# Performance work log

Measured on AMD Instinct MI355X. Metric: run time of the kernel, lower is better.

## Reference

```python
import jax, jax.numpy as jnp
import numpy as np

STRIDE = 4.0      # fpn_strides[0]
POOL = 7          # roi_align_size
SR = 2            # roi_align_sampling_ratio
NUM_CLASSES = 10
B, N = 2, 512
C, H, W = 256, 256, 256
OUT = 1024


def _bilinear(feat_hwc, y, x):
    # feat_hwc: [H, W, C]; y, x: [N, 7, 7, SR, SR] sample coords (feature units)
    Hf, Wf, _ = feat_hwc.shape
    valid = (y > -1.0) & (y < Hf) & (x > -1.0) & (x < Wf)
    y = jnp.clip(y, 0.0, Hf - 1.0)
    x = jnp.clip(x, 0.0, Wf - 1.0)
    y0 = jnp.floor(y)
    x0 = jnp.floor(x)
    y0i = y0.astype(jnp.int32)
    x0i = x0.astype(jnp.int32)
    y1i = jnp.minimum(y0i + 1, Hf - 1)
    x1i = jnp.minimum(x0i + 1, Wf - 1)
    ly = (y - y0)[..., None]
    lx = (x - x0)[..., None]
    hy = 1.0 - ly
    hx = 1.0 - lx
    v = (hy * hx * feat_hwc[y0i, x0i] + hy * lx * feat_hwc[y0i, x1i]
         + ly * hx * feat_hwc[y1i, x0i] + ly * lx * feat_hwc[y1i, x1i])
    return v * valid[..., None]


def _roi_align_rotated(feat_hwc, boxes):
    # boxes: [N, 5] = (cx, cy, w, h, theta) in feature coords -> [N, 7, 7, C]
    cx, cy, w, h, th = (boxes[:, k] for k in range(5))
    bins = jnp.arange(POOL, dtype=feat_hwc.dtype)
    sub = (jnp.arange(SR, dtype=feat_hwc.dtype) + 0.5) / SR
    # local (box-frame) coords of sample points along each axis: [N, 7, SR]
    ys = -h[:, None, None] / 2 + (h / POOL)[:, None, None] * (bins[None, :, None] + sub[None, None, :])
    xs = -w[:, None, None] / 2 + (w / POOL)[:, None, None] * (bins[None, :, None] + sub[None, None, :])
    yy = ys[:, :, None, :, None]  # [N,7,1,SR,1]
    xx = xs[:, None, :, None, :]  # [N,1,7,1,SR]
    cos = jnp.cos(th)[:, None, None, None, None]
    sin = jnp.sin(th)[:, None, None, None, None]
    gx = cx[:, None, None, None, None] + xx * cos - yy * sin
    gy = cy[:, None, None, None, None] + xx * sin + yy * cos
    v = _bilinear(feat_hwc, gy, gx)  # [N,7,7,SR,SR,C]
    return v.mean(axis=(3, 4))       # average-pool the SRxSR samples per bin


def norm_angle(a):
    return (a + jnp.pi / 2) % jnp.pi - jnp.pi / 2


def setup_inputs():
    key = jax.random.key(0)
    ks = jax.random.split(key, 14)
    feat = jax.random.normal(ks[0], (B, C, H, W), jnp.float32)
    cx = jax.random.uniform(ks[1], (B, N), minval=16.0, maxval=H - 16.0)
    cy = jax.random.uniform(ks[2], (B, N), minval=16.0, maxval=W - 16.0)
    bw = jax.random.uniform(ks[3], (B, N), minval=8.0, maxval=64.0)
    bh = jax.random.uniform(ks[4], (B, N), minval=8.0, maxval=64.0)
    th = jax.random.uniform(ks[5], (B, N), minval=-np.pi / 2, maxval=np.pi / 2)
    proposals = jnp.stack([cx, cy, bw, bh, th], axis=-1).astype(jnp.float32)
    d_in = C * POOL * POOL
    s = 0.02
    return {
        'feat': feat,
        'proposals': proposals,
        'W1': jax.random.normal(ks[6], (d_in, OUT), jnp.float32) * s,
        'b1': jnp.zeros((OUT,), jnp.float32),
        'W2': jax.random.normal(ks[7], (OUT, OUT), jnp.float32) * s,
        'b2': jnp.zeros((OUT,), jnp.float32),
        'Wcls': jax.random.normal(ks[8], (OUT, NUM_CLASSES + 1), jnp.float32) * s,
        'bcls': jnp.zeros((NUM_CLASSES + 1,), jnp.float32),
        'Wreg': jax.random.normal(ks[9], (OUT, 5), jnp.float32) * s,
        'breg': jnp.zeros((5,), jnp.float32),
    }


def reference(feat, proposals, W1, b1, W2, b2, Wcls, bcls, Wreg, breg):
    Bn, Nn = proposals.shape[:2]
    feat_hwc = jnp.transpose(feat, (0, 2, 3, 1))  # [B,H,W,C]
    pooled = jax.vmap(_roi_align_rotated)(feat_hwc, proposals)  # [B,N,7,7,C]
    # torch flattens [N, C, 7, 7] -> C*49; match that layout
    x = jnp.transpose(pooled, (0, 1, 4, 2, 3)).reshape(Bn, Nn, -1)
    x = jax.nn.relu(x @ W1 + b1)
    x = jax.nn.relu(x @ W2 + b2)
    cls = x @ Wcls + bcls   # [B,N,11]
    reg = x @ Wreg + breg   # [B,N,5]
    # decode (proposals scaled to image coords by stride; theta unscaled)
    scale = jnp.array([STRIDE, STRIDE, STRIDE, STRIDE, 1.0], feat.dtype)
    p = proposals * scale
    clamp_v = float(abs(np.log(16.0 / 1000.0)))
    bx = p[..., 2] * reg[..., 0] + p[..., 0]
    by = p[..., 3] * reg[..., 1] + p[..., 1]
    bw = p[..., 2] * jnp.exp(jnp.clip(reg[..., 2], -clamp_v, clamp_v))
    bh = p[..., 3] * jnp.exp(jnp.clip(reg[..., 3], -clamp_v, clamp_v))
    ba = norm_angle(p[..., 4] + reg[..., 4])
    boxes = jnp.stack([bx, by, bw, bh, ba], axis=-1)
    return boxes, cls
```

## Files before the change

kernel.cpp:

```cpp
#include <hip/hip_runtime.h>
#include <math.h>
#include <stdint.h>

#define BB 2
#define NN 512
#define CC 256
#define HH 256
#define WW 256
#define DIN 12544
#define OUT1 1024
#define NCLS 11
#define NROI 1024
#define SK1 8
#define SK2 2

typedef short bf16x8 __attribute__((ext_vector_type(8)));
typedef float f32x4 __attribute__((ext_vector_type(4)));

__device__ inline unsigned short f2bf(float f) {
  unsigned int u = __float_as_uint(f);
  u += 0x7FFF + ((u >> 16) & 1);
  return (unsigned short)(u >> 16);
}
__device__ inline float bf2f(unsigned short h) {
  return __uint_as_float(((unsigned int)h) << 16);
}
__device__ inline float4 ld_bf4(const unsigned short* p) {
  ushort4 r = *(const ushort4*)p;
  return make_float4(bf2f(r.x), bf2f(r.y), bf2f(r.z), bf2f(r.w));
}

__device__ inline void gll16(const void* g, void* l) {
  __builtin_amdgcn_global_load_lds(
      reinterpret_cast<const __attribute__((address_space(1))) void*>(
          reinterpret_cast<uintptr_t>(g)),
      reinterpret_cast<__attribute__((address_space(3))) void*>(
          (unsigned int)reinterpret_cast<uintptr_t>(l)),
      16, 0, 0);
}

__global__ __launch_bounds__(256) void prep_kernel(
    const float* __restrict__ feat, unsigned short* __restrict__ fhwc,
    const float* __restrict__ W1, unsigned short* __restrict__ W1T,
    const float* __restrict__ W2, unsigned short* __restrict__ W2T,
    int n_tr) {
  __shared__ float tile[8320];
  int bid = blockIdx.x;
  int tid = threadIdx.x;

  if (bid < n_tr) {
    int hw0 = (bid & 511) * 128;
    int c0 = ((bid >> 9) & 3) * 64;
    int b = bid >> 11;
    int cl_base = tid >> 5;
    int hwq = (tid & 31) * 4;
#pragma unroll
    for (int pass = 0; pass < 8; ++pass) {
      int cl = cl_base + pass * 8;
      float4 v = *(const float4*)(feat +
                                  ((size_t)b * CC + c0 + cl) * (HH * WW) +
                                  hw0 + hwq);
      tile[(hwq + 0) * 65 + cl] = v.x;
      tile[(hwq + 1) * 65 + cl] = v.y;
      tile[(hwq + 2) * 65 + cl] = v.z;
      tile[(hwq + 3) * 65 + cl] = v.w;
    }
    __syncthreads();
    int hi = tid >> 4, lo = tid & 15;
#pragma unroll
    for (int pass = 0; pass < 8; ++pass) {
      int hwl = hi + pass * 16;
      int cc = lo * 4;
      ushort4 o;
      o.x = f2bf(tile[hwl * 65 + cc + 0]);
      o.y = f2bf(tile[hwl * 65 + cc + 1]);
      o.z = f2bf(tile[hwl * 65 + cc + 2]);
      o.w = f2bf(tile[hwl * 65 + cc + 3]);
      *(ushort4*)(fhwc + ((size_t)b * (HH * WW) + hw0 + hwl) * CC + c0 + cc) =
          o;
    }
    return;
  }

  int u = bid - n_tr;
  const float* in;
  unsigned short* out;
  int Kout, kblk, nblk;
  bool perm;
  if (u < 1568) {
    in = W1; out = W1T; Kout = DIN; kblk = u % 196; nblk = u / 196; perm = true;
  } else {
    u -= 1568;
    in = W2; out = W2T; Kout = OUT1; kblk = u & 15; nblk = u >> 4; perm = false;
  }
  int k0 = kblk * 64, n0 = nblk * 128;
  int kl_base = tid >> 5;
  int nq = (tid & 31) * 4;
#pragma unroll
  for (int pass = 0; pass < 8; ++pass) {
    int kl = kl_base + pass * 8;
    int k = k0 + kl;
    int row = perm ? ((k & 255) * 49 + (k >> 8)) : k;
    float4 v = *(const float4*)(in + (size_t)row * OUT1 + n0 + nq);
    tile[kl * 129 + nq + 0] = v.x;
    tile[kl * 129 + nq + 1] = v.y;
    tile[kl * 129 + nq + 2] = v.z;
    tile[kl * 129 + nq + 3] = v.w;
  }
  __syncthreads();
  int hi = tid >> 4, lo = tid & 15;
#pragma unroll
  for (int pass = 0; pass < 8; ++pass) {
    int nl = hi + pass * 16;
    int kq = lo * 4;
    ushort4 o;
    o.x = f2bf(tile[(kq + 0) * 129 + nl]);
    o.y = f2bf(tile[(kq + 1) * 129 + nl]);
    o.z = f2bf(tile[(kq + 2) * 129 + nl]);
    o.w = f2bf(tile[(kq + 3) * 129 + nl]);
    *(ushort4*)(out + (size_t)(n0 + nl) * Kout + k0 + kq) = o;
  }
}

__device__ inline void bilin(float gy, float gx, int& y0, int& x0, int& y1,
                             int& x1, float& w00, float& w01, float& w10,
                             float& w11) {
  float valid = (gy > -1.f && gy < 256.f && gx > -1.f && gx < 256.f) ? 0.25f : 0.f;
  float y = fminf(fmaxf(gy, 0.f), 255.f);
  float x = fminf(fmaxf(gx, 0.f), 255.f);
  float yf = floorf(y), xf = floorf(x);
  y0 = (int)yf; x0 = (int)xf;
  y1 = min(y0 + 1, 255); x1 = min(x0 + 1, 255);
  float ly = y - yf, lx = x - xf, hy = 1.f - ly, hx = 1.f - lx;
  w00 = hy * hx * valid; w01 = hy * lx * valid;
  w10 = ly * hx * valid; w11 = ly * lx * valid;
}

__global__ __launch_bounds__(256) void roi_align_hwc(
    const unsigned short* __restrict__ fhwc, const float* __restrict__ props,
    unsigned short* __restrict__ pooled) {
  int roi = blockIdx.x >> 1;
  int half = blockIdx.x & 1;
  int b = roi >> 9;
  const float* p = props + (size_t)roi * 5;
  float cx = p[0], cy = p[1], w = p[2], h = p[3], th = p[4];
  float sn = sinf(th), cs = cosf(th);
  int wave = threadIdx.x >> 6, lane = threadIdx.x & 63;
  int c4 = lane * 4;
  const unsigned short* fb = fhwc + (size_t)b * HH * WW * CC;
  unsigned short* outp = pooled + (size_t)roi * DIN;

  for (int bin = half * 4 + wave; bin < 49; bin += 8) {
    int py = bin / 7, px = bin - py * 7;
    float a0 = 0.f, a1 = 0.f, a2 = 0.f, a3 = 0.f;
#pragma unroll
    for (int sy = 0; sy < 2; ++sy) {
#pragma unroll
      for (int sx = 0; sx < 2; ++sx) {
        float ys = -0.5f * h + (h / 7.0f) * ((float)py + ((float)sy + 0.5f) * 0.5f);
        float xs = -0.5f * w + (w / 7.0f) * ((float)px + ((float)sx + 0.5f) * 0.5f);
        float gx = cx + xs * cs - ys * sn;
        float gy = cy + xs * sn + ys * cs;
        int y0, x0, y1, x1; float w00, w01, w10, w11;
        bilin(gy, gx, y0, x0, y1, x1, w00, w01, w10, w11);
        float4 v00 = ld_bf4(fb + ((size_t)(y0 * WW + x0)) * CC + c4);
        float4 v01 = ld_bf4(fb + ((size_t)(y0 * WW + x1)) * CC + c4);
        float4 v10 = ld_bf4(fb + ((size_t)(y1 * WW + x0)) * CC + c4);
        float4 v11 = ld_bf4(fb + ((size_t)(y1 * WW + x1)) * CC + c4);
        a0 += w00 * v00.x + w01 * v01.x + w10 * v10.x + w11 * v11.x;
        a1 += w00 * v00.y + w01 * v01.y + w10 * v10.y + w11 * v11.y;
        a2 += w00 * v00.z + w01 * v01.z + w10 * v10.z + w11 * v11.z;
        a3 += w00 * v00.w + w01 * v01.w + w10 * v10.w + w11 * v11.w;
      }
    }
    ushort4 o;
    o.x = f2bf(a0); o.y = f2bf(a1); o.z = f2bf(a2); o.w = f2bf(a3);
    *(ushort4*)(outp + bin * 256 + c4) = o;
  }
}

__global__ __launch_bounds__(256) void roi_align_nchw(
    const float* __restrict__ feat, const float* __restrict__ props,
    unsigned short* __restrict__ pooled) {
  int roi = blockIdx.x;
  int b = roi >> 9;
  int c = threadIdx.x;
  const float* p = props + (size_t)roi * 5;
  float cx = p[0], cy = p[1], w = p[2], h = p[3], th = p[4];
  float sn = sinf(th), cs = cosf(th);
  const float* fb = feat + ((size_t)b * CC + c) * (HH * WW);
  unsigned short* outp = pooled + (size_t)roi * DIN;
  for (int bin = 0; bin < 49; ++bin) {
    int py = bin / 7, px = bin - py * 7;
    float acc = 0.f;
#pragma unroll
    for (int sy = 0; sy < 2; ++sy) {
#pragma unroll
      for (int sx = 0; sx < 2; ++sx) {
        float ys = -0.5f * h + (h / 7.0f) * ((float)py + ((float)sy + 0.5f) * 0.5f);
        float xs = -0.5f * w + (w / 7.0f) * ((float)px + ((float)sx + 0.5f) * 0.5f);
        float gx = cx + xs * cs - ys * sn;
        float gy = cy + xs * sn + ys * cs;
        int y0, x0, y1, x1; float w00, w01, w10, w11;
        bilin(gy, gx, y0, x0, y1, x1, w00, w01, w10, w11);
        acc += w00 * fb[(size_t)y0 * WW + x0] + w01 * fb[(size_t)y0 * WW + x1] +
               w10 * fb[(size_t)y1 * WW + x0] + w11 * fb[(size_t)y1 * WW + x1];
      }
    }
    outp[bin * 256 + c] = f2bf(acc);
  }
}

__global__ __launch_bounds__(256) void gemm_mfma_128(
    const unsigned short* __restrict__ A, const unsigned short* __restrict__ Bw,
    float* __restrict__ part, int K, int Ks) {
  __shared__ short As[128 * 32];
  __shared__ short Bs[128 * 32];
  int tid = threadIdx.x;
  int w = tid >> 6, lane = tid & 63;
  int quad = lane >> 4, l16 = lane & 15;
  int m0 = blockIdx.y * 128, n0 = blockIdx.x * 128;
  int bz = blockIdx.z;
  int wm = w >> 1, wn = w & 1;

  const char* pA = (const char*)A +
      ((size_t)(m0 + 32 * w + (lane >> 2)) * K + (size_t)bz * Ks) * 2 +
      (lane & 3) * 16;
  const char* pB = (const char*)Bw +
      ((size_t)(n0 + 32 * w + (lane >> 2)) * K + (size_t)bz * Ks) * 2 +
      (lane & 3) * 16;
  short* la = &As[w * 1024];
  short* lb = &Bs[w * 1024];
  const size_t rstep = (size_t)K * 2 * 16;

  f32x4 acc[4][4] = {};
  int aoff[4], boff[4];
#pragma unroll
  for (int t = 0; t < 4; ++t) {
    aoff[t] = (wm * 64 + t * 16 + l16) * 32 + quad * 8;
    boff[t] = (wn * 64 + t * 16 + l16) * 32 + quad * 8;
  }

  for (int kk = 0; kk < Ks; kk += 32) {
    __syncthreads();
    gll16(pA, la);
    gll16(pA + rstep, la + 512);
    gll16(pB, lb);
    gll16(pB + rstep, lb + 512);
    pA += 64; pB += 64;
    __syncthreads();
    bf16x8 af[4], bfr[4];
#pragma unroll
    for (int t = 0; t < 4; ++t) af[t] = *(const bf16x8*)&As[aoff[t]];
#pragma unroll
    for (int t = 0; t < 4; ++t) bfr[t] = *(const bf16x8*)&Bs[boff[t]];
#pragma unroll
    for (int mt = 0; mt < 4; ++mt)
#pragma unroll
      for (int nt = 0; nt < 4; ++nt)
        acc[mt][nt] = __builtin_amdgcn_mfma_f32_16x16x32_bf16(
            af[mt], bfr[nt], acc[mt][nt], 0, 0, 0);
  }

  float* pp = part + (size_t)bz * (OUT1 * NROI);
#pragma unroll
  for (int mt = 0; mt < 4; ++mt)
#pragma unroll
    for (int nt = 0; nt < 4; ++nt) {
      int col = n0 + wn * 64 + nt * 16 + l16;
#pragma unroll
      for (int r = 0; r < 4; ++r) {
        int row = m0 + wm * 64 + mt * 16 + quad * 4 + r;
        pp[(size_t)row * OUT1 + col] = acc[mt][nt][r];
      }
    }
}

__global__ __launch_bounds__(256) void reduce_relu_bf16(
    const float* __restrict__ part, const float* __restrict__ bias,
    unsigned short* __restrict__ out) {
  int i = blockIdx.x * 256 + threadIdx.x;
  int base = i * 4;
  int col = base & (OUT1 - 1);
  const float4* p = (const float4*)part;
  float4 s = p[i];
#pragma unroll
  for (int z = 1; z < SK1; ++z) {
    float4 t = p[i + (size_t)z * (NROI * OUT1 / 4)];
    s.x += t.x; s.y += t.y; s.z += t.z; s.w += t.w;
  }
  float4 bv = *(const float4*)(bias + col);
  ushort4 o;
  o.x = f2bf(fmaxf(s.x + bv.x, 0.f));
  o.y = f2bf(fmaxf(s.y + bv.y, 0.f));
  o.z = f2bf(fmaxf(s.z + bv.z, 0.f));
  o.w = f2bf(fmaxf(s.w + bv.w, 0.f));
  *(ushort4*)(out + base) = o;
}

__global__ __launch_bounds__(256) void gemm_mfma_64_part(
    const unsigned short* __restrict__ A, const unsigned short* __restrict__ Bw,
    float* __restrict__ part, int K, int Ks) {
  __shared__ short As[64 * 64];
  __shared__ short Bs[64 * 64];
  int tid = threadIdx.x;
  int w = tid >> 6, lane = tid & 63;
  int quad = lane >> 4, l16 = lane & 15;
  int m0 = blockIdx.y * 64, n0 = blockIdx.x * 64;
  int bz = blockIdx.z;
  int wm = w >> 1, wn = w & 1;

  const char* pA = (const char*)A +
      ((size_t)(m0 + 16 * w + (lane >> 3)) * K + (size_t)bz * Ks) * 2 +
      (lane & 7) * 16;
  const char* pB = (const char*)Bw +
      ((size_t)(n0 + 16 * w + (lane >> 3)) * K + (size_t)bz * Ks) * 2 +
      (lane & 7) * 16;
  short* la = &As[w * 1024];
  short* lb = &Bs[w * 1024];
  const size_t rstep = (size_t)K * 2 * 8;

  f32x4 acc[2][2] = {};
  int aoff[2], boff[2];
#pragma unroll
  for (int t = 0; t < 2; ++t) {
    aoff[t] = (wm * 32 + t * 16 + l16) * 64 + quad * 8;
    boff[t] = (wn * 32 + t * 16 + l16) * 64 + quad * 8;
  }

  for (int kk = 0; kk < Ks; kk += 64) {
    __syncthreads();
    gll16(pA, la);
    gll16(pA + rstep, la + 512);
    gll16(pB, lb);
    gll16(pB + rstep, lb + 512);
    pA += 128; pB += 128;
    __syncthreads();
#pragma unroll
    for (int ks = 0; ks < 2; ++ks) {
      bf16x8 af[2], bfr[2];
#pragma unroll
      for (int t = 0; t < 2; ++t) af[t] = *(const bf16x8*)&As[aoff[t] + ks * 32];
#pragma unroll
      for (int t = 0; t < 2; ++t) bfr[t] = *(const bf16x8*)&Bs[boff[t] + ks * 32];
#pragma unroll
      for (int mt = 0; mt < 2; ++mt)
#pragma unroll
        for (int nt = 0; nt < 2; ++nt)
          acc[mt][nt] = __builtin_amdgcn_mfma_f32_16x16x32_bf16(
              af[mt], bfr[nt], acc[mt][nt], 0, 0, 0);
    }
  }
  float* pp = part + (size_t)bz * (OUT1 * NROI);
#pragma unroll
  for (int mt = 0; mt < 2; ++mt)
#pragma unroll
    for (int nt = 0; nt < 2; ++nt) {
      int col = n0 + wn * 32 + nt * 16 + l16;
#pragma unroll
      for (int r = 0; r < 4; ++r) {
        int row = m0 + wm * 32 + mt * 16 + quad * 4 + r;
        pp[(size_t)row * OUT1 + col] = acc[mt][nt][r];
      }
    }
}

__global__ __launch_bounds__(256) void head_kernel(
    const float* __restrict__ P0, const float* __restrict__ P1,
    const float* __restrict__ b2, const float* __restrict__ Wcls,
    const float* __restrict__ bcls, const float* __restrict__ Wreg,
    const float* __restrict__ breg, const float* __restrict__ props,
    float* __restrict__ out) {
  __shared__ float xrow[1024];
  __shared__ float partial[16][17];
  __shared__ float res[16];
  int row = blockIdx.x;
  int tid = threadIdx.x;
  {
    size_t off = (size_t)row * 1024 + tid * 4;
    float4 a = *(const float4*)(P0 + off);
    float4 b = *(const float4*)(P1 + off);
    float4 bv = *(const float4*)(b2 + tid * 4);
    xrow[tid * 4 + 0] = fmaxf(a.x + b.x + bv.x, 0.f);
    xrow[tid * 4 + 1] = fmaxf(a.y + b.y + bv.y, 0.f);
    xrow[tid * 4 + 2] = fmaxf(a.z + b.z + bv.z, 0.f);
    xrow[tid * 4 + 3] = fmaxf(a.w + b.w + bv.w, 0.f);
  }
  __syncthreads();
  int col = tid & 15, slice = tid >> 4;
  float s = 0.f;
  if (col < NCLS) {
    for (int k = slice * 64; k < slice * 64 + 64; ++k)
      s += xrow[k] * Wcls[(size_t)k * NCLS + col];
  } else {
    int rc = col - NCLS;
    for (int k = slice * 64; k < slice * 64 + 64; ++k)
      s += xrow[k] * Wreg[(size_t)k * 5 + rc];
  }
  partial[slice][col] = s;
  __syncthreads();
  if (tid < 16) {
    float t = 0.f;
    for (int sl = 0; sl < 16; ++sl) t += partial[sl][tid];
    t += (tid < NCLS) ? bcls[tid] : breg[tid - NCLS];
    res[tid] = t;
  }
  __syncthreads();
  if (tid < NCLS) out[5120 + (size_t)row * NCLS + tid] = res[tid];
  if (tid == 0) {
    const float* p = props + (size_t)row * 5;
    float p0 = p[0] * 4.f, p1 = p[1] * 4.f, p2 = p[2] * 4.f, p3 = p[3] * 4.f,
          p4 = p[4];
    float r0 = res[11], r1 = res[12], r2 = res[13], r3 = res[14], r4 = res[15];
    const float V = 4.135166556742356f;
    float bx = p2 * r0 + p0;
    float by = p3 * r1 + p1;
    float bw = p2 * expf(fminf(fmaxf(r2, -V), V));
    float bh = p3 * expf(fminf(fmaxf(r3, -V), V));
    const float PI = 3.14159265358979323846f;
    float a = p4 + r4;
    float m = fmodf(a + PI * 0.5f, PI);
    if (m < 0.f) m += PI;
    float ba = m - PI * 0.5f;
    float* bo = out + (size_t)row * 5;
    bo[0] = bx; bo[1] = by; bo[2] = bw; bo[3] = bh; bo[4] = ba;
  }
}

extern "C" void kernel_launch(void* const* d_in, const int* in_sizes, int n_in,
                              void* d_out, int out_size, void* d_ws,
                              size_t ws_size, hipStream_t stream) {
  const float* feat  = (const float*)d_in[0];
  const float* props = (const float*)d_in[1];
  const float* W1    = (const float*)d_in[2];
  const float* b1    = (const float*)d_in[3];
  const float* W2    = (const float*)d_in[4];
  const float* b2    = (const float*)d_in[5];
  const float* Wcls  = (const float*)d_in[6];
  const float* bcls  = (const float*)d_in[7];
  const float* Wreg  = (const float*)d_in[8];
  const float* breg  = (const float*)d_in[9];
  float* out = (float*)d_out;

  char* wp = (char*)d_ws;
  unsigned short* pooled = (unsigned short*)wp; wp += (size_t)NROI * DIN * 2;
  unsigned short* W1T    = (unsigned short*)wp; wp += (size_t)OUT1 * DIN * 2;
  unsigned short* W2T    = (unsigned short*)wp; wp += (size_t)OUT1 * OUT1 * 2;
  unsigned short* x1     = (unsigned short*)wp; wp += (size_t)NROI * OUT1 * 2;
  float*          part1  = (float*)wp;          wp += (size_t)SK1 * NROI * OUT1 * 4;
  float*          part2  = (float*)wp;          wp += (size_t)SK2 * NROI * OUT1 * 4;
  unsigned short* fhwc   = (unsigned short*)wp;

  size_t need_min  = (size_t)(wp - (char*)d_ws);
  size_t need_full = need_min + (size_t)BB * CC * HH * WW * 2;

  int n_tr = (ws_size >= need_full) ? (BB * 4 * (HH * WW / 128)) : 0;
  int n_prep = n_tr + 1568 + 128;

  prep_kernel<<<n_prep, 256, 0, stream>>>(feat, fhwc, W1, W1T, W2, W2T, n_tr);

  if (n_tr) {
    roi_align_hwc<<<NROI * 2, 256, 0, stream>>>(fhwc, props, pooled);
  } else {
    roi_align_nchw<<<NROI, 256, 0, stream>>>(feat, props, pooled);
  }

  gemm_mfma_128<<<dim3(8, 8, SK1), 256, 0, stream>>>(pooled, W1T, part1, DIN,
                                                     DIN / SK1);
  reduce_relu_bf16<<<NROI * OUT1 / 1024, 256, 0, stream>>>(part1, b1, x1);
  gemm_mfma_64_part<<<dim3(16, 16, SK2), 256, 0, stream>>>(x1, W2T, part2, OUT1,
                                                           OUT1 / SK2);
  head_kernel<<<NROI, 256, 0, stream>>>(part2, part2 + (size_t)NROI * OUT1, b2,
                                        Wcls, bcls, Wreg, breg, props, out);
}
```

Before: 386.3 us.

## Move weight transposes into ROI-align kernel and shrink transpose tiles to bf16

The feature NCHW-to-HWC transpose now runs in its own kernel, and the W1/W2 transpose-and-convert blocks are merged into the ROI-align launch as extra leading blocks. The weight conversion can then overlap with the gather-heavy ROI sampling instead of sharing a launch with the feature transpose. The transpose tiles also convert to bf16 before staging in LDS, halving shared memory per block, which may allow more resident blocks. The risk is that ROI blocks wait behind the weight blocks scheduled ahead of them, and the tile padding may cause LDS bank conflicts on the strided column reads.

Result: no change. 384.6 us (-0.5%).

```diff
diff --git a/kernel.cpp b/kernel.cpp
--- a/kernel.cpp
+++ b/kernel.cpp
@@ -13,6 +13,7 @@
 #define NROI 1024
 #define SK1 8
 #define SK2 2
+#define NWB 1696
 
 typedef short bf16x8 __attribute__((ext_vector_type(8)));
 typedef float f32x4 __attribute__((ext_vector_type(4)));
@@ -39,86 +40,37 @@
       16, 0, 0);
 }
 
-__global__ __launch_bounds__(256) void prep_kernel(
-    const float* __restrict__ feat, unsigned short* __restrict__ fhwc,
-    const float* __restrict__ W1, unsigned short* __restrict__ W1T,
-    const float* __restrict__ W2, unsigned short* __restrict__ W2T,
-    int n_tr) {
-  __shared__ float tile[8320];
+__global__ __launch_bounds__(256) void prep_feat(
+    const float* __restrict__ feat, unsigned short* __restrict__ fhwc) {
+  __shared__ unsigned short tile[64 * 132];
   int bid = blockIdx.x;
   int tid = threadIdx.x;
-
-  if (bid < n_tr) {
-    int hw0 = (bid & 511) * 128;
-    int c0 = ((bid >> 9) & 3) * 64;
-    int b = bid >> 11;
-    int cl_base = tid >> 5;
-    int hwq = (tid & 31) * 4;
-#pragma unroll
-    for (int pass = 0; pass < 8; ++pass) {
-      int cl = cl_base + pass * 8;
-      float4 v = *(const float4*)(feat +
-                                  ((size_t)b * CC + c0 + cl) * (HH * WW) +
-                                  hw0 + hwq);
-      tile[(hwq + 0) * 65 + cl] = v.x;
-      tile[(hwq + 1) * 65 + cl] = v.y;
-      tile[(hwq + 2) * 65 + cl] = v.z;
-      tile[(hwq + 3) * 65 + cl] = v.w;
-    }
-    __syncthreads();
-    int hi = tid >> 4, lo = tid & 15;
-#pragma unroll
-    for (int pass = 0; pass < 8; ++pass) {
-      int hwl = hi + pass * 16;
-      int cc = lo * 4;
-      ushort4 o;
-      o.x = f2bf(tile[hwl * 65 + cc + 0]);
-      o.y = f2bf(tile[hwl * 65 + cc + 1]);
-      o.z = f2bf(tile[hwl * 65 + cc + 2]);
-      o.w = f2bf(tile[hwl * 65 + cc + 3]);
-      *(ushort4*)(fhwc + ((size_t)b * (HH * WW) + hw0 + hwl) * CC + c0 + cc) =
-          o;
-    }
-    return;
-  }
-
-  int u = bid - n_tr;
-  const float* in;
-  unsigned short* out;
-  int Kout, kblk, nblk;
-  bool perm;
-  if (u < 1568) {
-    in = W1; out = W1T; Kout = DIN; kblk = u % 196; nblk = u / 196; perm = true;
-  } else {
-    u -= 1568;
-    in = W2; out = W2T; Kout = OUT1; kblk = u & 15; nblk = u >> 4; perm = false;
-  }
-  int k0 = kblk * 64, n0 = nblk * 128;
-  int kl_base = tid >> 5;
-  int nq = (tid & 31) * 4;
+  int hw0 = (bid & 511) * 128;
+  int c0 = ((bid >> 9) & 3) * 64;
+  int b = bid >> 11;
+  int cl_base = tid >> 5;
+  int hwq = (tid & 31) * 4;
 #pragma unroll
   for (int pass = 0; pass < 8; ++pass) {
-    int kl = kl_base + pass * 8;
-    int k = k0 + kl;
-    int row = perm ? ((k & 255) * 49 + (k >> 8)) : k;
-    float4 v = *(const float4*)(in + (size_t)row * OUT1 + n0 + nq);
-    tile[kl * 129 + nq + 0] = v.x;
-    tile[kl * 129 + nq + 1] = v.y;
-    tile[kl * 129 + nq + 2] = v.z;
-    tile[kl * 129 + nq + 3] = v.w;
+    int cl = cl_base + pass * 8;
+    float4 v = *(const float4*)(feat + ((size_t)b * CC + c0 + cl) * (HH * WW) +
+                                hw0 + hwq);
+    ushort4 o;
+    o.x = f2bf(v.x); o.y = f2bf(v.y); o.z = f2bf(v.z); o.w = f2bf(v.w);
+    *(ushort4*)&tile[cl * 132 + hwq] = o;
   }
   __syncthreads();
   int hi = tid >> 4, lo = tid & 15;
 #pragma unroll
   for (int pass = 0; pass < 8; ++pass) {
-    int nl = hi + pass * 16;
-    int kq = lo * 4;
+    int hwl = hi + pass * 16;
+    int cq = lo * 4;
     ushort4 o;
-    o.x = f2bf(tile[(kq + 0) * 129 + nl]);
-    o.y = f2bf(tile[(kq + 1) * 129 + nl]);
-    o.z = f2bf(tile[(kq + 2) * 129 + nl]);
-    o.w = f2bf(tile[(kq + 3) * 129 + nl]);
-    *(ushort4*)(out + (size_t)(n0 + nl) * Kout + k0 + kq) = o;
+    o.x = tile[(cq + 0) * 132 + hwl];
+    o.y = tile[(cq + 1) * 132 + hwl];
+    o.z = tile[(cq + 2) * 132 + hwl];
+    o.w = tile[(cq + 3) * 132 + hwl];
+    *(ushort4*)(fhwc + ((size_t)b * (HH * WW) + hw0 + hwl) * CC + c0 + cq) = o;
   }
 }
 
@@ -136,16 +88,66 @@
   w10 = ly * hx * valid; w11 = ly * lx * valid;
 }
 
-__global__ __launch_bounds__(256) void roi_align_hwc(
+__global__ __launch_bounds__(256) void roi_fused(
     const unsigned short* __restrict__ fhwc, const float* __restrict__ props,
-    unsigned short* __restrict__ pooled) {
-  int roi = blockIdx.x >> 1;
-  int half = blockIdx.x & 1;
+    unsigned short* __restrict__ pooled, const float* __restrict__ W1,
+    unsigned short* __restrict__ W1T, const float* __restrict__ W2,
+    unsigned short* __restrict__ W2T) {
+  __shared__ unsigned short tile[64 * 132];
+  int bid = blockIdx.x;
+  int tid = threadIdx.x;
+
+  if (bid < NWB) {
+    int u = bid;
+    const float* in;
+    unsigned short* out;
+    int Kout, kblk, nblk;
+    bool perm;
+    if (u < 1568) {
+      in = W1; out = W1T; Kout = DIN; kblk = u % 196; nblk = u / 196;
+      perm = true;
+    } else {
+      u -= 1568;
+      in = W2; out = W2T; Kout = OUT1; kblk = u & 15; nblk = u >> 4;
+      perm = false;
+    }
+    int k0 = kblk * 64, n0 = nblk * 128;
+    int kl_base = tid >> 5;
+    int nq = (tid & 31) * 4;
+#pragma unroll
+    for (int pass = 0; pass < 8; ++pass) {
+      int kl = kl_base + pass * 8;
+      int k = k0 + kl;
+      int row = perm ? ((k & 255) * 49 + (k >> 8)) : k;
+      float4 v = *(const float4*)(in + (size_t)row * OUT1 + n0 + nq);
+      ushort4 o;
+      o.x = f2bf(v.x); o.y = f2bf(v.y); o.z = f2bf(v.z); o.w = f2bf(v.w);
+      *(ushort4*)&tile[kl * 132 + nq] = o;
+    }
+    __syncthreads();
+    int hi = tid >> 4, lo = tid & 15;
+#pragma unroll
+    for (int pass = 0; pass < 8; ++pass) {
+      int nl = hi + pass * 16;
+      int kq = lo * 4;
+      ushort4 o;
+      o.x = tile[(kq + 0) * 132 + nl];
+      o.y = tile[(kq + 1) * 132 + nl];
+      o.z = tile[(kq + 2) * 132 + nl];
+      o.w = tile[(kq + 3) * 132 + nl];
+      *(ushort4*)(out + (size_t)(n0 + nl) * Kout + k0 + kq) = o;
+    }
+    return;
+  }
+
+  int rb = bid - NWB;
+  int roi = rb >> 1;
+  int half = rb & 1;
   int b = roi >> 9;
   const float* p = props + (size_t)roi * 5;
   float cx = p[0], cy = p[1], w = p[2], h = p[3], th = p[4];
   float sn = sinf(th), cs = cosf(th);
-  int wave = threadIdx.x >> 6, lane = threadIdx.x & 63;
+  int wave = tid >> 6, lane = tid & 63;
   int c4 = lane * 4;
   const unsigned short* fb = fhwc + (size_t)b * HH * WW * CC;
   unsigned short* outp = pooled + (size_t)roi * DIN;
@@ -454,14 +456,12 @@
   size_t need_min  = (size_t)(wp - (char*)d_ws);
   size_t need_full = need_min + (size_t)BB * CC * HH * WW * 2;
 
-  int n_tr = (ws_size >= need_full) ? (BB * 4 * (HH * WW / 128)) : 0;
-  int n_prep = n_tr + 1568 + 128;
-
-  prep_kernel<<<n_prep, 256, 0, stream>>>(feat, fhwc, W1, W1T, W2, W2T, n_tr);
-
-  if (n_tr) {
-    roi_align_hwc<<<NROI * 2, 256, 0, stream>>>(fhwc, props, pooled);
+  if (ws_size >= need_full) {
+    prep_feat<<<BB * 4 * (HH * WW / 128), 256, 0, stream>>>(feat, fhwc);
+    roi_fused<<<NWB + NROI * 2, 256, 0, stream>>>(fhwc, props, pooled, W1, W1T,
+                                                  W2, W2T);
   } else {
+    roi_fused<<<NWB, 256, 0, stream>>>(fhwc, props, pooled, W1, W1T, W2, W2T);
     roi_align_nchw<<<NROI, 256, 0, stream>>>(feat, props, pooled);
   }
 
```
